# Kernel optimization log

Hardware: AMD Instinct MI355X
Metric: run time of the kernel (lower is better)

Reference implementation:

```python
import jax, jax.numpy as jnp
import numpy as np

B, T, N, D, H, F, L, V = 4, 512, 1024, 384, 8, 1536, 6, 8000
HD = D // H


def _pe(t, d):
    pos = np.arange(t)[:, None].astype(np.float32)
    div = np.exp(np.arange(0, d, 2).astype(np.float32) * (-np.log(10000.0) / d))
    pe = np.zeros((t, d), np.float32)
    pe[:, 0::2] = np.sin(pos * div)
    pe[:, 1::2] = np.cos(pos * div)
    return jnp.asarray(pe)


def _ln(x, g, b, eps=1e-5):
    m = jnp.mean(x, -1, keepdims=True)
    v = jnp.mean((x - m) ** 2, -1, keepdims=True)
    return (x - m) * jax.lax.rsqrt(v + eps) * g + b


def _mha(xq, xkv, qw, qb, kw, kb, vw, vb, ow, ob, causal):
    Bq, Tq, Dm = xq.shape
    Nk = xkv.shape[1]

    def proj(x, w, b):
        return (x @ w + b).reshape(x.shape[0], x.shape[1], H, HD).transpose(0, 2, 1, 3)

    q, k, v = proj(xq, qw, qb), proj(xkv, kw, kb), proj(xkv, vw, vb)
    s = jnp.einsum('bhtd,bhnd->bhtn', q, k) * (HD ** -0.5)
    if causal:  # triu(ones(T, T_total), diagonal=1) since T_total == T (no cache)
        mask = jnp.triu(jnp.ones((Tq, Nk), bool), 1)
        s = jnp.where(mask, -jnp.inf, s)
    p = jax.nn.softmax(s, -1)
    o = jnp.einsum('bhtn,bhnd->bhtd', p, v).transpose(0, 2, 1, 3).reshape(Bq, Tq, Dm)
    return o @ ow + ob


def setup_inputs() -> dict:
    key = jax.random.key(0)
    ks = iter(jax.random.split(key, 40))
    w = lambda shape, s=0.02: jax.random.normal(next(ks), shape, jnp.float32) * s
    inp = {
        'encoder_out': jax.random.normal(next(ks), (B, N, D), jnp.float32),
        'emb': w((V, D)),
    }
    for p in ('sa', 'ca'):
        for n in ('q', 'k', 'v', 'o'):
            inp[f'{p}_{n}w'] = w((L, D, D))
            inp[f'{p}_{n}b'] = jnp.zeros((L, D), jnp.float32)
    for n in ('ln1', 'ln2', 'ln3'):
        inp[f'{n}_g'] = jnp.ones((L, D), jnp.float32)
        inp[f'{n}_b'] = jnp.zeros((L, D), jnp.float32)
    inp['ffn_w1'] = w((L, D, F)); inp['ffn_b1'] = jnp.zeros((L, F), jnp.float32)
    inp['ffn_w2'] = w((L, F, D)); inp['ffn_b2'] = jnp.zeros((L, D), jnp.float32)
    inp['on_g'] = jnp.ones((D,), jnp.float32); inp['on_b'] = jnp.zeros((D,), jnp.float32)
    inp['out_w'] = w((D, V)); inp['out_b'] = jnp.zeros((V,), jnp.float32)
    inp['target_ids'] = jax.random.randint(next(ks), (B, T), 0, V)
    return inp


def _forward(encoder_out, emb, sa_qw, sa_qb, sa_kw, sa_kb, sa_vw, sa_vb, sa_ow, sa_ob,
             ca_qw, ca_qb, ca_kw, ca_kb, ca_vw, ca_vb, ca_ow, ca_ob,
             ln1_g, ln1_b, ln2_g, ln2_b, ln3_g, ln3_b,
             ffn_w1, ffn_b1, ffn_w2, ffn_b2, on_g, on_b, out_w, out_b, target_ids):
    x = emb[target_ids] + _pe(T, D)[None]  # [B,T,D]
    for i in range(L):
        a = _mha(x, x, sa_qw[i], sa_qb[i], sa_kw[i], sa_kb[i], sa_vw[i], sa_vb[i], sa_ow[i], sa_ob[i], True)
        x = _ln(x + a, ln1_g[i], ln1_b[i])
        c = _mha(x, encoder_out, ca_qw[i], ca_qb[i], ca_kw[i], ca_kb[i], ca_vw[i], ca_vb[i], ca_ow[i], ca_ob[i], False)
        x = _ln(x + c, ln2_g[i], ln2_b[i])
        h = jax.nn.gelu(x @ ffn_w1[i] + ffn_b1[i], approximate=False) @ ffn_w2[i] + ffn_b2[i]
        x = _ln(x + h, ln3_g[i], ln3_b[i])
    x = _ln(x, on_g, on_b)
    return x @ out_w + out_b  # logits [B,T,V]


def reference(encoder_out, emb, sa_qw, sa_qb, sa_kw, sa_kb, sa_vw, sa_vb, sa_ow, sa_ob,
              ca_qw, ca_qb, ca_kw, ca_kb, ca_vw, ca_vb, ca_ow, ca_ob,
              ln1_g, ln1_b, ln2_g, ln2_b, ln3_g, ln3_b,
              ffn_w1, ffn_b1, ffn_w2, ffn_b2, on_g, on_b, out_w, out_b, target_ids):
    return _forward(encoder_out, emb, sa_qw, sa_qb, sa_kw, sa_kb, sa_vw, sa_vb, sa_ow, sa_ob,
                    ca_qw, ca_qb, ca_kw, ca_kb, ca_vw, ca_vb, ca_ow, ca_ob,
                    ln1_g, ln1_b, ln2_g, ln2_b, ln3_g, ln3_b,
                    ffn_w1, ffn_b1, ffn_w2, ffn_b2, on_g, on_b, out_w, out_b, target_ids)
```

## Files before the change

### kernel.cpp

```cpp
#include <hip/hip_runtime.h>
#include <hip/hip_bf16.h>
#include <math.h>

typedef __hip_bfloat16 bf16;
typedef __attribute__((ext_vector_type(8))) short short8;
typedef __attribute__((ext_vector_type(4))) float f32x4;
typedef __attribute__((ext_vector_type(4))) unsigned short us4;

#define Bc 4
#define Tc 512
#define Nc 1024
#define Dc 384
#define Hc 8
#define Fc 1536
#define Lc 6
#define Vc 8000
#define HDc 48

__device__ __forceinline__ float ldsel(const void* p, long long i, int isbf) {
  return isbf ? __bfloat162float(((const bf16*)p)[i]) : ((const float*)p)[i];
}
__device__ __forceinline__ void stsel(void* p, long long i, float v, int isbf) {
  if (isbf) ((bf16*)p)[i] = __float2bfloat16(v);
  else      ((float*)p)[i] = v;
}
__device__ __forceinline__ unsigned short f2bf(float x) {
  unsigned int u = __float_as_uint(x);
  return (unsigned short)((u + 0x7fffu + ((u >> 16) & 1u)) >> 16);
}

__device__ __forceinline__ int xcd_swz(int d, int nwg) {
  const int q = nwg >> 3, r = nwg & 7;
  const int x = d & 7, idx = d >> 3;
  return (x < r) ? x * (q + 1) + idx : r * (q + 1) + (x - r) * q + idx;
}

__global__ void detect_kernel(const unsigned int* __restrict__ g,
                              int* __restrict__ flag) {
  if (threadIdx.x == 0 && blockIdx.x == 0)
    *flag = (g[0] == 0x3F803F80u) ? 1 : 0;
}

__global__ __launch_bounds__(256) void wt_kernel(
    const void* __restrict__ in, bf16* __restrict__ out, int K, int N,
    long long outStride, const int* __restrict__ flagp) {
  const int isbf = *flagp;
  __shared__ float t[32][33];
  const long long cin = (long long)blockIdx.z * K * N;
  const long long cout = (long long)blockIdx.z * outStride;
  const int n0 = blockIdx.x * 32, k0 = blockIdx.y * 32;
  const int tx = threadIdx.x, ty = threadIdx.y;
#pragma unroll
  for (int r = 0; r < 4; ++r)
    t[ty * 4 + r][tx] =
        ldsel(in, cin + (long long)(k0 + ty * 4 + r) * N + n0 + tx, isbf);
  __syncthreads();
#pragma unroll
  for (int r = 0; r < 4; ++r)
    out[cout + (long long)(n0 + ty * 4 + r) * K + k0 + tx] =
        __float2bfloat16(t[tx][ty * 4 + r]);
}

__global__ __launch_bounds__(256) void cvt_kernel(
    const void* __restrict__ in, bf16* __restrict__ out,
    const int* __restrict__ flagp) {
  const int isbf = *flagp;
  const long long i = ((long long)blockIdx.x * 256 + threadIdx.x) * 4;
  if (isbf) {
    *(us4*)((unsigned short*)out + i) = *(const us4*)((const unsigned short*)in + i);
  } else {
    float4 v = *(const float4*)((const float*)in + i);
    unsigned short* o = (unsigned short*)out + i;
    o[0] = f2bf(v.x); o[1] = f2bf(v.y); o[2] = f2bf(v.z); o[3] = f2bf(v.w);
  }
}

__global__ __launch_bounds__(256) void bfuse_kernel(
    const void* __restrict__ b0, const void* __restrict__ b1,
    const void* __restrict__ b2, float* __restrict__ out, int nseg,
    const int* __restrict__ flagp) {
  const int isbf = *flagp;
  const int i = blockIdx.x;
  for (int n = threadIdx.x; n < Dc; n += 256) {
    out[(long long)i * nseg * Dc + n] = ldsel(b0, (long long)i * Dc + n, isbf);
    if (nseg > 1)
      out[(long long)i * nseg * Dc + Dc + n] = ldsel(b1, (long long)i * Dc + n, isbf);
    if (nseg > 2)
      out[(long long)i * nseg * Dc + 2 * Dc + n] = ldsel(b2, (long long)i * Dc + n, isbf);
  }
}

template <int BN>
__global__ __launch_bounds__(256) void mgemm128_kernel(
    const bf16* __restrict__ A, const bf16* __restrict__ Bt, long long bOff,
    const void* __restrict__ bias, long long biasOff, void* __restrict__ C,
    int M, int N, int K, int cMode, int act, int biasBf,
    const int* __restrict__ flagp) {
  constexpr int RN = BN / 32;
  const int isbf = *flagp;
  const int cbf = (cMode == 2) ? isbf : cMode;
  const int bbf = (biasBf == 2) ? isbf : biasBf;

  __shared__ __align__(16) unsigned short As[128][72];
  __shared__ __align__(16) unsigned short Bs[BN][72];

  const int tid = threadIdx.x;
  const int gx = gridDim.x;
  const int wl = xcd_swz(blockIdx.y * gx + blockIdx.x, gx * gridDim.y);
  const int m0 = (wl % gx) * 128, n0 = (wl / gx) * BN;
  const int lane = tid & 63, wv = tid >> 6;
  const int wm = wv >> 1, wn = wv & 1;
  const int fr = lane & 15;
  const int fk = (lane >> 4) * 8;

  const int ar = tid >> 3;
  const int ac = (tid & 7) * 8;
  const bf16* Ap = A + (long long)(m0 + ar) * K + ac;
  const bf16* Bp_r[RN * 2];
#pragma unroll
  for (int r = 0; r < RN * 2; ++r) {
    int rn = n0 + ar + 32 * r;
    rn = (rn < N) ? rn : (N - 1);
    Bp_r[r] = Bt + bOff + (long long)rn * K + ac;
  }

  short8 pa[4], pb[RN * 2];
#pragma unroll
  for (int r = 0; r < 4; ++r) pa[r] = *(const short8*)(Ap + r * 32 * K);
#pragma unroll
  for (int r = 0; r < RN * 2; ++r) pb[r] = *(const short8*)(Bp_r[r]);

  f32x4 acc[4][RN] = {};

  for (int k0 = 0; k0 < K; k0 += 64) {
#pragma unroll
    for (int r = 0; r < 4; ++r) *(short8*)(&As[ar + 32 * r][ac]) = pa[r];
#pragma unroll
    for (int r = 0; r < RN * 2; ++r) *(short8*)(&Bs[ar + 32 * r][ac]) = pb[r];
    __syncthreads();
    if (k0 + 64 < K) {
#pragma unroll
      for (int r = 0; r < 4; ++r)
        pa[r] = *(const short8*)(Ap + r * 32 * K + k0 + 64);
#pragma unroll
      for (int r = 0; r < RN * 2; ++r)
        pb[r] = *(const short8*)(Bp_r[r] + k0 + 64);
    }
#pragma unroll
    for (int ks = 0; ks < 64; ks += 32) {
      short8 af[4];
#pragma unroll
      for (int mi = 0; mi < 4; ++mi)
        af[mi] = *(const short8*)(&As[wm * 64 + mi * 16 + fr][ks + fk]);
      short8 bg[RN];
#pragma unroll
      for (int ni = 0; ni < RN; ++ni)
        bg[ni] = *(const short8*)(&Bs[wn * (BN / 2) + ni * 16 + fr][ks + fk]);
#pragma unroll
      for (int mi = 0; mi < 4; ++mi)
#pragma unroll
        for (int ni = 0; ni < RN; ++ni)
          acc[mi][ni] =
              __builtin_amdgcn_mfma_f32_16x16x32_bf16(af[mi], bg[ni], acc[mi][ni], 0, 0, 0);
    }
    __syncthreads();
  }

#pragma unroll
  for (int ni = 0; ni < RN; ++ni) {
    const int col = n0 + wn * (BN / 2) + ni * 16 + fr;
    if (col >= N) continue;
    const float bv = bias ? ldsel(bias, biasOff + col, bbf) : 0.f;
#pragma unroll
    for (int mi = 0; mi < 4; ++mi) {
#pragma unroll
      for (int q = 0; q < 4; ++q) {
        const int row = m0 + wm * 64 + mi * 16 + (lane >> 4) * 4 + q;
        float v = acc[mi][ni][q] + bv;
        if (act == 1) v = 0.5f * v * (1.f + erff(v * 0.70710678118654752f));
        stsel(C, (long long)row * N + col, v, cbf);
      }
    }
  }
}

__global__ __launch_bounds__(256) void mgemm_kernel(
    const bf16* __restrict__ A, const void* __restrict__ B, long long bOff,
    const void* __restrict__ bias, long long biasOff, void* __restrict__ C,
    int M, int N, int K, int cMode, int act, int biasBf, int bT,
    const int* __restrict__ flagp) {
  const int isbf = *flagp;
  const int cbf = (cMode == 2) ? isbf : cMode;
  const int bbf = (biasBf == 2) ? isbf : biasBf;

  __shared__ __align__(16) unsigned short As[64][72];
  __shared__ __align__(16) unsigned short Bs[64][72];

  const int tid = threadIdx.x;
  const int gx = gridDim.x;
  const int wl = xcd_swz(blockIdx.y * gx + blockIdx.x, gx * gridDim.y);
  const int m0 = (wl % gx) * 64, n0 = (wl / gx) * 64;
  const int lane = tid & 63, wv = tid >> 6;
  const int fr = lane & 15;
  const int fk = (lane >> 4) * 8;

  const int sr = tid >> 2;
  const int sk = (tid & 3) * 16;

  f32x4 acc[4] = {};

  if (bT == 0) {
    const bf16* Bp = (const bf16*)B + bOff;
    const bf16* Ar = A + (long long)(m0 + sr) * K + sk;
    const bf16* Br = Bp + (long long)(n0 + sr) * K + sk;
    short8 a0 = *(const short8*)(Ar);
    short8 a1 = *(const short8*)(Ar + 8);
    short8 b0 = *(const short8*)(Br);
    short8 b1 = *(const short8*)(Br + 8);
    for (int k0 = 0; k0 < K; k0 += 64) {
      *(short8*)(&As[sr][sk]) = a0;
      *(short8*)(&As[sr][sk + 8]) = a1;
      *(short8*)(&Bs[sr][sk]) = b0;
      *(short8*)(&Bs[sr][sk + 8]) = b1;
      __syncthreads();
      if (k0 + 64 < K) {
        a0 = *(const short8*)(Ar + k0 + 64);
        a1 = *(const short8*)(Ar + k0 + 72);
        b0 = *(const short8*)(Br + k0 + 64);
        b1 = *(const short8*)(Br + k0 + 72);
      }
#pragma unroll
      for (int ks = 0; ks < 64; ks += 32) {
        short8 a = *(const short8*)(&As[16 * wv + fr][ks + fk]);
#pragma unroll
        for (int j = 0; j < 4; ++j) {
          short8 b = *(const short8*)(&Bs[16 * j + fr][ks + fk]);
          acc[j] = __builtin_amdgcn_mfma_f32_16x16x32_bf16(a, b, acc[j], 0, 0, 0);
        }
      }
      __syncthreads();
    }
  } else {
    const int bk = tid >> 2;
    const int bn = (tid & 3) * 16;
    for (int k0 = 0; k0 < K; k0 += 64) {
      {
        const long long off = (long long)(m0 + sr) * K + k0 + sk;
        const short8* p = (const short8*)(A + off);
        *(short8*)(&As[sr][sk]) = p[0];
        *(short8*)(&As[sr][sk + 8]) = p[1];
      }
      const long long off = bOff + (long long)(k0 + bk) * N + n0 + bn;
      if (isbf) {
        const short8* p = (const short8*)((const bf16*)B + off);
        short8 v0 = p[0], v1 = p[1];
#pragma unroll
        for (int j = 0; j < 8; ++j) {
          Bs[bn + j][bk] = (unsigned short)v0[j];
          Bs[bn + 8 + j][bk] = (unsigned short)v1[j];
        }
      } else {
        const float4* p = (const float4*)((const float*)B + off);
        float4 f0 = p[0], f1 = p[1], f2 = p[2], f3 = p[3];
        Bs[bn + 0][bk] = f2bf(f0.x);  Bs[bn + 1][bk] = f2bf(f0.y);
        Bs[bn + 2][bk] = f2bf(f0.z);  Bs[bn + 3][bk] = f2bf(f0.w);
        Bs[bn + 4][bk] = f2bf(f1.x);  Bs[bn + 5][bk] = f2bf(f1.y);
        Bs[bn + 6][bk] = f2bf(f1.z);  Bs[bn + 7][bk] = f2bf(f1.w);
        Bs[bn + 8][bk] = f2bf(f2.x);  Bs[bn + 9][bk] = f2bf(f2.y);
        Bs[bn + 10][bk] = f2bf(f2.z); Bs[bn + 11][bk] = f2bf(f2.w);
        Bs[bn + 12][bk] = f2bf(f3.x); Bs[bn + 13][bk] = f2bf(f3.y);
        Bs[bn + 14][bk] = f2bf(f3.z); Bs[bn + 15][bk] = f2bf(f3.w);
      }
      __syncthreads();
#pragma unroll
      for (int ks = 0; ks < 64; ks += 32) {
        short8 a = *(const short8*)(&As[16 * wv + fr][ks + fk]);
#pragma unroll
        for (int j = 0; j < 4; ++j) {
          short8 b = *(const short8*)(&Bs[16 * j + fr][ks + fk]);
          acc[j] = __builtin_amdgcn_mfma_f32_16x16x32_bf16(a, b, acc[j], 0, 0, 0);
        }
      }
      __syncthreads();
    }
  }

#pragma unroll
  for (int j = 0; j < 4; ++j) {
    const int col = n0 + 16 * j + fr;
    float bv = bias ? ldsel(bias, biasOff + col, bbf) : 0.f;
#pragma unroll
    for (int q = 0; q < 4; ++q) {
      const int row = m0 + 16 * wv + (lane >> 4) * 4 + q;
      float v = acc[j][q] + bv;
      if (act == 1) v = 0.5f * v * (1.f + erff(v * 0.70710678118654752f));
      stsel(C, (long long)row * N + col, v, cbf);
    }
  }
}

__global__ __launch_bounds__(256) void mattn_kernel(
    const bf16* __restrict__ Qb, int ldq, const bf16* __restrict__ Kb,
    const bf16* __restrict__ Vb, int ldkv, int kvRows,
    float* __restrict__ PO, float* __restrict__ Mb, float* __restrict__ Lb,
    int Nk, int causal) {
  const int bh = blockIdx.y;
  const int b = bh >> 3, h = bh & 7;
  const int row0 = blockIdx.x * 64;
  const int z = blockIdx.z;
  const int tid = threadIdx.x;
  const int lane = tid & 63, wv = tid >> 6;
  const int fr = lane & 15, g = lane >> 4;
  const int fk = g * 8, g4 = g * 4;
  const int rbase = row0 + wv * 16 + g4;

  __shared__ __align__(16) unsigned short Ks[64][72];
  __shared__ __align__(16) unsigned short Vt[48][72];
  __shared__ __align__(16) unsigned short Ps[4][16][72];

  for (int i = tid; i < 64 * 16; i += 256) Ks[i >> 4][48 + (i & 15)] = 0;

  const int qrow = row0 + wv * 16 + fr;
  const bf16* Qp = Qb + (long long)(b * Tc + qrow) * ldq + h * HDc;
  short8 q0 = *(const short8*)(Qp + fk);
  short8 q1 = {};
  if (g < 2) q1 = *(const short8*)(Qp + 32 + fk);

  const bf16* Kp = Kb + (long long)b * kvRows * ldkv + h * HDc;
  const bf16* Vp = Vb + (long long)b * kvRows * ldkv + h * HDc;

  const int c0 = tid, c1 = 256 + tid;
  const int r0 = c0 / 6, o0 = (c0 % 6) * 8;
  const int r1 = c1 / 6, o1 = (c1 % 6) * 8;
  const bool has1 = (tid < 128);

  const int nT = causal ? (blockIdx.x + 1) : (Nk >> 6);
  const int tlo = (nT * z) >> 1, thi = (nT * (z + 1)) >> 1;

  float m[4] = {-3e38f, -3e38f, -3e38f, -3e38f};
  float l[4] = {0.f, 0.f, 0.f, 0.f};
  f32x4 oa[3] = {};

  short8 kA = {}, vA = {}, kB = {}, vB = {};
  if (tlo < thi) {
    const long long nb = (long long)tlo * 64;
    kA = *(const short8*)(Kp + (nb + r0) * ldkv + o0);
    vA = *(const short8*)(Vp + (nb + r0) * ldkv + o0);
    if (has1) {
      kB = *(const short8*)(Kp + (nb + r1) * ldkv + o1);
      vB = *(const short8*)(Vp + (nb + r1) * ldkv + o1);
    }
  }

  const float scale = 0.20823509f;

  for (int t = tlo; t < thi; ++t) {
    *(short8*)&Ks[r0][o0] = kA;
#pragma unroll
    for (int j = 0; j < 8; ++j) Vt[o0 + j][r0] = (unsigned short)vA[j];
    if (has1) {
      *(short8*)&Ks[r1][o1] = kB;
#pragma unroll
      for (int j = 0; j < 8; ++j) Vt[o1 + j][r1] = (unsigned short)vB[j];
    }
    __syncthreads();

    if (t + 1 < thi) {
      const long long nb = (long long)(t + 1) * 64;
      kA = *(const short8*)(Kp + (nb + r0) * ldkv + o0);
      vA = *(const short8*)(Vp + (nb + r0) * ldkv + o0);
      if (has1) {
        kB = *(const short8*)(Kp + (nb + r1) * ldkv + o1);
        vB = *(const short8*)(Vp + (nb + r1) * ldkv + o1);
      }
    }

    f32x4 s[4] = {};
#pragma unroll
    for (int tt = 0; tt < 4; ++tt) {
      short8 b0 = *(const short8*)&Ks[16 * tt + fr][fk];
      short8 b1 = *(const short8*)&Ks[16 * tt + fr][32 + fk];
      s[tt] = __builtin_amdgcn_mfma_f32_16x16x32_bf16(q0, b0, s[tt], 0, 0, 0);
      s[tt] = __builtin_amdgcn_mfma_f32_16x16x32_bf16(q1, b1, s[tt], 0, 0, 0);
    }

    const int n0 = t * 64;
#pragma unroll
    for (int tt = 0; tt < 4; ++tt) {
      const int n = n0 + 16 * tt + fr;
#pragma unroll
      for (int q = 0; q < 4; ++q) {
        float v = s[tt][q] * scale;
        if (causal && n > rbase + q) v = -3e38f;
        s[tt][q] = v;
      }
    }

#pragma unroll
    for (int q = 0; q < 4; ++q) {
      float tm = fmaxf(fmaxf(s[0][q], s[1][q]), fmaxf(s[2][q], s[3][q]));
      tm = fmaxf(tm, __shfl_xor(tm, 1, 64));
      tm = fmaxf(tm, __shfl_xor(tm, 2, 64));
      tm = fmaxf(tm, __shfl_xor(tm, 4, 64));
      tm = fmaxf(tm, __shfl_xor(tm, 8, 64));
      const float mn = fmaxf(m[q], tm);
      const float f = exp2f(m[q] - mn);
      float rs = 0.f;
#pragma unroll
      for (int tt = 0; tt < 4; ++tt) {
        float p = exp2f(s[tt][q] - mn);
        s[tt][q] = p;
        rs += p;
      }
      rs += __shfl_xor(rs, 1, 64);
      rs += __shfl_xor(rs, 2, 64);
      rs += __shfl_xor(rs, 4, 64);
      rs += __shfl_xor(rs, 8, 64);
      l[q] = l[q] * f + rs;
      m[q] = mn;
      oa[0][q] *= f;
      oa[1][q] *= f;
      oa[2][q] *= f;
    }

#pragma unroll
    for (int tt = 0; tt < 4; ++tt)
#pragma unroll
      for (int q = 0; q < 4; ++q)
        Ps[wv][g4 + q][16 * tt + fr] = f2bf(s[tt][q]);

#pragma unroll
    for (int ks = 0; ks < 64; ks += 32) {
      short8 a = *(const short8*)&Ps[wv][fr][ks + fk];
#pragma unroll
      for (int jd = 0; jd < 3; ++jd) {
        short8 bv = *(const short8*)&Vt[16 * jd + fr][ks + fk];
        oa[jd] = __builtin_amdgcn_mfma_f32_16x16x32_bf16(a, bv, oa[jd], 0, 0, 0);
      }
    }
    __syncthreads();
  }

#pragma unroll
  for (int q = 0; q < 4; ++q) {
    float* pp = PO + (long long)(z * (Bc * Tc) + b * Tc + rbase + q) * Dc + h * HDc;
#pragma unroll
    for (int jd = 0; jd < 3; ++jd) pp[16 * jd + fr] = oa[jd][q];
    if (fr == 0) {
      const int mi = z * (Bc * Hc * Tc) + (bh << 9) + rbase + q;
      Mb[mi] = m[q];
      Lb[mi] = l[q];
    }
  }
}

__global__ __launch_bounds__(384) void acomb_kernel(
    const float* __restrict__ PO, const float* __restrict__ Mb,
    const float* __restrict__ Lb, bf16* __restrict__ ATT) {
  const int row = blockIdx.x;
  const int d = threadIdx.x;
  const int b = row >> 9, t = row & 511;
  const int h = d / HDc;
  const int mi = ((b << 3) + h) * Tc + t;
  const float m0 = Mb[mi], m1 = Mb[Bc * Hc * Tc + mi];
  const float l0 = Lb[mi], l1 = Lb[Bc * Hc * Tc + mi];
  const float M = fmaxf(m0, m1);
  const float w0 = exp2f(m0 - M), w1 = exp2f(m1 - M);
  const float L = w0 * l0 + w1 * l1;
  const float o = (w0 * PO[(long long)row * Dc + d] +
                   w1 * PO[(long long)(Bc * Tc + row) * Dc + d]) / L;
  ATT[(long long)row * Dc + d] = __float2bfloat16(o);
}

__global__ __launch_bounds__(256) void lnw_kernel(
    const float* __restrict__ X, const float* __restrict__ R,
    const void* __restrict__ g, const void* __restrict__ bta, long long gOff,
    void* __restrict__ Y, int yMode, bf16* __restrict__ Yb,
    const int* __restrict__ flagp) {
  const int isbf = *flagp;
  const long long row = blockIdx.x * 4 + (threadIdx.x >> 6);
  const int lane = threadIdx.x & 63;
  const float* xr = X + row * Dc;
  const float* rr = R ? R + row * Dc : nullptr;
  float v[6];
  float s = 0.f, s2 = 0.f;
#pragma unroll
  for (int j = 0; j < 6; ++j) {
    const int d = lane + 64 * j;
    float x = xr[d] + (rr ? rr[d] : 0.f);
    v[j] = x; s += x; s2 += x * x;
  }
#pragma unroll
  for (int k = 1; k < 64; k <<= 1) {
    s += __shfl_xor(s, k, 64);
    s2 += __shfl_xor(s2, k, 64);
  }
  const float mean = s * (1.f / 384.f);
  const float var = s2 * (1.f / 384.f) - mean * mean;
  const float rstd = rsqrtf(var + 1e-5f);
  const long long yo = row * Dc;
#pragma unroll
  for (int j = 0; j < 6; ++j) {
    const int d = lane + 64 * j;
    float y = (v[j] - mean) * rstd * ldsel(g, gOff + d, isbf) +
              ldsel(bta, gOff + d, isbf);
    stsel(Y, yo + d, y, yMode);
    if (Yb) Yb[yo + d] = __float2bfloat16(y);
  }
}

__global__ __launch_bounds__(384) void embed_kernel(
    const void* __restrict__ emb, const int* __restrict__ ids,
    float* __restrict__ X, bf16* __restrict__ Xb,
    const int* __restrict__ flagp) {
  const int isbf = *flagp;
  long long row = blockIdx.x;
  int t = (int)(row % Tc);
  int d = threadIdx.x;
  int id = ids[row];
  float e = ldsel(emb, (long long)id * Dc + d, isbf);
  int i2 = d & ~1;
  float div = expf((float)i2 * (-9.210340371976184f / 384.f));
  float ang = (float)t * div;
  float pe = (d & 1) ? cosf(ang) : sinf(ang);
  float v = e + pe;
  X[row * Dc + d] = v;
  Xb[row * Dc + d] = __float2bfloat16(v);
}

extern "C" void kernel_launch(void* const* d_in, const int* in_sizes, int n_in,
                              void* d_out, int out_size, void* d_ws,
                              size_t ws_size, hipStream_t stream) {
  (void)in_sizes; (void)n_in; (void)out_size;

  const void* enc = d_in[0];
  const void* emb = d_in[1];
  const void* sa_w[4]; const void* sa_b[4];
  for (int j = 0; j < 4; ++j) { sa_w[j] = d_in[2 + 2 * j]; sa_b[j] = d_in[3 + 2 * j]; }
  const void* ca_w[4]; const void* ca_b[4];
  for (int j = 0; j < 4; ++j) { ca_w[j] = d_in[10 + 2 * j]; ca_b[j] = d_in[11 + 2 * j]; }
  const void* ln_g[3]; const void* ln_b[3];
  for (int j = 0; j < 3; ++j) { ln_g[j] = d_in[18 + 2 * j]; ln_b[j] = d_in[19 + 2 * j]; }
  const void* fw1 = d_in[24];
  const void* fb1 = d_in[25];
  const void* fw2 = d_in[26];
  const void* fb2 = d_in[27];
  const void* ong = d_in[28];
  const void* onb = d_in[29];
  const void* outw = d_in[30];
  const void* outb = d_in[31];
  const int* ids = (const int*)d_in[32];

  char* ob = (char*)d_out;
  float* X   = (float*)ob;
  bf16* Xb   = (bf16*)(ob + 3145728);
  float* AO  = (float*)(ob + 4718592);
  bf16* QKV  = (bf16*)(ob + 7864320);
  bf16* KVca = (bf16*)(ob + 12582912);
  bf16* ATT  = (bf16*)(ob + 18874368);
  bf16* HID  = (bf16*)(ob + 20447232);
  float* PO  = (float*)(ob + 20447232);
  float* Mb  = (float*)(ob + 26738688);
  float* Lb  = (float*)(ob + 26869760);
  bf16* encB = (bf16*)(ob + 27000832);
  float* bQKV = (float*)(ob + 30146560);
  float* bKVc = (float*)(ob + 30174208);

  bf16* Y = (bf16*)d_ws;
  int* flag = (int*)((char*)d_ws + 1572864);

  const bool bigws = (ws_size >= (size_t)36028672);
  char* wtb = (char*)d_ws + 1573120;
  bf16* saQKVT = (bf16*)(wtb + 0);
  bf16* saOT   = (bf16*)(wtb + 5308416);
  bf16* caQT   = (bf16*)(wtb + 7077888);
  bf16* caKVT  = (bf16*)(wtb + 8847360);
  bf16* caOT   = (bf16*)(wtb + 12386304);
  bf16* f1T    = (bf16*)(wtb + 14155776);
  bf16* f2T    = (bf16*)(wtb + 21233664);
  bf16* outT   = (bf16*)(wtb + 28311552);

  const int BT = Bc * Tc;
  const int F32 = 0, BF16 = 1, FLAG = 2;

  detect_kernel<<<dim3(1), dim3(64), 0, stream>>>((const unsigned int*)ln_g[0], flag);

  if (bigws) {
    auto wt = [&](const void* in, bf16* out, int K, int N, long long ostr, int C) {
      wt_kernel<<<dim3(N / 32, K / 32, C), dim3(32, 8), 0, stream>>>(
          in, out, K, N, ostr, flag);
    };
    wt(sa_w[0], saQKVT, 384, 384, 1152LL * 384, Lc);
    wt(sa_w[1], saQKVT + 147456, 384, 384, 1152LL * 384, Lc);
    wt(sa_w[2], saQKVT + 294912, 384, 384, 1152LL * 384, Lc);
    wt(sa_w[3], saOT, 384, 384, 147456, Lc);
    wt(ca_w[0], caQT, 384, 384, 147456, Lc);
    wt(ca_w[1], caKVT, 384, 384, 294912, Lc);
    wt(ca_w[2], caKVT + 147456, 384, 384, 294912, Lc);
    wt(ca_w[3], caOT, 384, 384, 147456, Lc);
    wt(fw1, f1T, 384, 1536, 589824, Lc);
    wt(fw2, f2T, 1536, 384, 589824, Lc);
    wt(outw, outT, 384, 8000, 0, 1);
    bfuse_kernel<<<dim3(Lc), dim3(256), 0, stream>>>(sa_b[0], sa_b[1], sa_b[2],
                                                     bQKV, 3, flag);
    bfuse_kernel<<<dim3(Lc), dim3(256), 0, stream>>>(ca_b[1], ca_b[2], ca_b[2],
                                                     bKVc, 2, flag);
  }
  cvt_kernel<<<dim3(1536), dim3(256), 0, stream>>>(enc, encB, flag);

  auto gemmBig = [&](const bf16* A, const bf16* Bt, long long bOff,
                     const void* bias, long long biasOff, int biasBf, void* C,
                     int M, int N, int K, int cM, int act) {
    mgemm128_kernel<128>
        <<<dim3(M / 128, (N + 127) / 128), dim3(256), 0, stream>>>(
            A, Bt, bOff, bias, biasOff, C, M, N, K, cM, act, biasBf, flag);
  };
  auto gemmT = [&](const bf16* A, const bf16* Bt, long long bOff,
                   const void* bias, long long biasOff, int biasBf, void* C,
                   int M, int N, int K, int cM, int act) {
    mgemm_kernel<<<dim3(M / 64, N / 64), dim3(256), 0, stream>>>(
        A, Bt, bOff, bias, biasOff, C, M, N, K, cM, act, biasBf, 0, flag);
  };
  auto gemmO = [&](const bf16* A, const void* Bo, long long bOff,
                   const void* bias, long long biasOff, void* C,
                   int M, int N, int K, int cM, int act) {
    mgemm_kernel<<<dim3(M / 64, N / 64), dim3(256), 0, stream>>>(
        A, Bo, bOff, bias, biasOff, C, M, N, K, cM, act, FLAG, 1, flag);
  };
  auto ln = [&](const float* Xp, const float* Rp, const void* g,
                const void* b, long long gOff, void* Yp, int yMode, bf16* Yb) {
    lnw_kernel<<<dim3(BT / 4), dim3(256), 0, stream>>>(Xp, Rp, g, b, gOff, Yp,
                                                       yMode, Yb, flag);
  };
  auto attn = [&](const bf16* Q, int ldq, const bf16* Kp, const bf16* Vp,
                  int ldkv, int kvRows, int Nk, int causal) {
    mattn_kernel<<<dim3(Tc / 64, Bc * Hc, 2), dim3(256), 0, stream>>>(
        Q, ldq, Kp, Vp, ldkv, kvRows, PO, Mb, Lb, Nk, causal);
    acomb_kernel<<<dim3(BT), dim3(384), 0, stream>>>(PO, Mb, Lb, ATT);
  };

  embed_kernel<<<dim3(BT), dim3(384), 0, stream>>>(emb, ids, X, Xb, flag);

  bf16* Qf = QKV;
  bf16* Kf = KVca;
  bf16* Vf = (bf16*)((char*)KVca + 3145728);

  for (int i = 0; i < Lc; ++i) {
    const long long wD = (long long)i * Dc * Dc;
    const long long bD = (long long)i * Dc;

    if (bigws) {
      gemmT(Xb, saQKVT, (long long)i * 1152 * 384, bQKV, (long long)i * 1152,
            F32, QKV, BT, 1152, 384, BF16, 0);
      attn(QKV, 1152, QKV + 384, QKV + 768, 1152, Tc, Tc, 1);
      gemmT(ATT, saOT, wD, sa_b[3], bD, FLAG, AO, BT, Dc, Dc, F32, 0);
    } else {
      gemmO(Xb, sa_w[0], wD, sa_b[0], bD, Qf, BT, Dc, Dc, BF16, 0);
      gemmO(Xb, sa_w[1], wD, sa_b[1], bD, Kf, BT, Dc, Dc, BF16, 0);
      gemmO(Xb, sa_w[2], wD, sa_b[2], bD, Vf, BT, Dc, Dc, BF16, 0);
      attn(Qf, 384, Kf, Vf, 384, Tc, Tc, 1);
      gemmO(ATT, sa_w[3], wD, sa_b[3], bD, AO, BT, Dc, Dc, F32, 0);
    }
    ln(X, AO, ln_g[0], ln_b[0], bD, X, F32, Xb);

    if (bigws) {
      gemmT(Xb, caQT, wD, ca_b[0], bD, FLAG, QKV, BT, Dc, Dc, BF16, 0);
      gemmT(encB, caKVT, (long long)i * 768 * 384, bKVc, (long long)i * 768,
            F32, KVca, Bc * Nc, 768, 384, BF16, 0);
      attn(QKV, 384, KVca, KVca + 384, 768, Nc, Nc, 0);
      gemmT(ATT, caOT, wD, ca_b[3], bD, FLAG, AO, BT, Dc, Dc, F32, 0);
    } else {
      gemmO(Xb, ca_w[0], wD, ca_b[0], bD, Qf, BT, Dc, Dc, BF16, 0);
      gemmO(encB, ca_w[1], wD, ca_b[1], bD, Kf, Bc * Nc, Dc, Dc, BF16, 0);
      gemmO(encB, ca_w[2], wD, ca_b[2], bD, Vf, Bc * Nc, Dc, Dc, BF16, 0);
      attn(Qf, 384, Kf, Vf, 384, Nc, Nc, 0);
      gemmO(ATT, ca_w[3], wD, ca_b[3], bD, AO, BT, Dc, Dc, F32, 0);
    }
    ln(X, AO, ln_g[1], ln_b[1], bD, X, F32, Xb);

    if (bigws) {
      gemmT(Xb, f1T, (long long)i * 1536 * 384, fb1, (long long)i * Fc, FLAG,
            HID, BT, Fc, Dc, BF16, 1 );
      gemmT(HID, f2T, (long long)i * 384 * 1536, fb2, bD, FLAG, AO,
            BT, Dc, Fc, F32, 0);
    } else {
      gemmO(Xb, fw1, (long long)i * Dc * Fc, fb1, (long long)i * Fc, HID,
            BT, Fc, Dc, BF16, 1);
      gemmO(HID, fw2, (long long)i * Fc * Dc, fb2, bD, AO, BT, Dc, Fc, F32, 0);
    }
    ln(X, AO, ln_g[2], ln_b[2], bD, X, F32, Xb);
  }

  ln(X, nullptr, ong, onb, 0, Y, BF16, nullptr);
  if (bigws)
    gemmBig(Y, outT, 0, outb, 0, FLAG, d_out, BT, Vc, Dc, FLAG, 0);
  else
    gemmO(Y, outw, 0, outb, 0, d_out, BT, Vc, Dc, FLAG, 0);
}
```

Baseline: 1.070 ms.

## Split-K narrow GEMMs, 4-way attention KV split, smaller output GEMM tile

Adds split-K to the 64x64 GEMM kernel through Klen/Ktot/kOff parameters. The N=384 projection and FFN-down GEMMs become two half-K launches into separate fp32 buffers, and the layernorm kernel sums both partials. Attention now splits the KV range four ways instead of two, with partials stored in reused scratch slots and a 4-way combine. The vocab GEMM switches to a 64-wide N tile to launch more blocks. The aim is better CU occupancy for small grids, at the cost of extra launches, more fp32 partial traffic and more scratch-buffer aliasing.

```diff
diff --git a/kernel.cpp b/kernel.cpp
--- a/kernel.cpp
+++ b/kernel.cpp
@@ -187,8 +187,8 @@
 __global__ __launch_bounds__(256) void mgemm_kernel(
     const bf16* __restrict__ A, const void* __restrict__ B, long long bOff,
     const void* __restrict__ bias, long long biasOff, void* __restrict__ C,
-    int M, int N, int K, int cMode, int act, int biasBf, int bT,
-    const int* __restrict__ flagp) {
+    int M, int N, int Klen, int Ktot, int kOff, int cMode, int act, int biasBf,
+    int bT, const int* __restrict__ flagp) {
   const int isbf = *flagp;
   const int cbf = (cMode == 2) ? isbf : cMode;
   const int bbf = (biasBf == 2) ? isbf : biasBf;
@@ -211,19 +211,19 @@
 
   if (bT == 0) {
     const bf16* Bp = (const bf16*)B + bOff;
-    const bf16* Ar = A + (long long)(m0 + sr) * K + sk;
-    const bf16* Br = Bp + (long long)(n0 + sr) * K + sk;
+    const bf16* Ar = A + (long long)(m0 + sr) * Ktot + kOff + sk;
+    const bf16* Br = Bp + (long long)(n0 + sr) * Ktot + kOff + sk;
     short8 a0 = *(const short8*)(Ar);
     short8 a1 = *(const short8*)(Ar + 8);
     short8 b0 = *(const short8*)(Br);
     short8 b1 = *(const short8*)(Br + 8);
-    for (int k0 = 0; k0 < K; k0 += 64) {
+    for (int k0 = 0; k0 < Klen; k0 += 64) {
       *(short8*)(&As[sr][sk]) = a0;
       *(short8*)(&As[sr][sk + 8]) = a1;
       *(short8*)(&Bs[sr][sk]) = b0;
       *(short8*)(&Bs[sr][sk + 8]) = b1;
       __syncthreads();
-      if (k0 + 64 < K) {
+      if (k0 + 64 < Klen) {
         a0 = *(const short8*)(Ar + k0 + 64);
         a1 = *(const short8*)(Ar + k0 + 72);
         b0 = *(const short8*)(Br + k0 + 64);
@@ -243,14 +243,14 @@
   } else {
     const int bk = tid >> 2;
     const int bn = (tid & 3) * 16;
-    for (int k0 = 0; k0 < K; k0 += 64) {
+    for (int k0 = 0; k0 < Klen; k0 += 64) {
       {
-        const long long off = (long long)(m0 + sr) * K + k0 + sk;
+        const long long off = (long long)(m0 + sr) * Ktot + kOff + k0 + sk;
         const short8* p = (const short8*)(A + off);
         *(short8*)(&As[sr][sk]) = p[0];
         *(short8*)(&As[sr][sk + 8]) = p[1];
       }
-      const long long off = bOff + (long long)(k0 + bk) * N + n0 + bn;
+      const long long off = bOff + (long long)(kOff + k0 + bk) * N + n0 + bn;
       if (isbf) {
         const short8* p = (const short8*)((const bf16*)B + off);
         short8 v0 = p[0], v1 = p[1];
@@ -302,7 +302,8 @@
 __global__ __launch_bounds__(256) void mattn_kernel(
     const bf16* __restrict__ Qb, int ldq, const bf16* __restrict__ Kb,
     const bf16* __restrict__ Vb, int ldkv, int kvRows,
-    float* __restrict__ PO, float* __restrict__ Mb, float* __restrict__ Lb,
+    float* __restrict__ P0s, float* __restrict__ P1s, float* __restrict__ P2s,
+    float* __restrict__ P3s, float* __restrict__ Mb, float* __restrict__ Lb,
     int Nk, int causal) {
   const int bh = blockIdx.y;
   const int b = bh >> 3, h = bh & 7;
@@ -335,7 +336,7 @@
   const bool has1 = (tid < 128);
 
   const int nT = causal ? (blockIdx.x + 1) : (Nk >> 6);
-  const int tlo = (nT * z) >> 1, thi = (nT * (z + 1)) >> 1;
+  const int tlo = (nT * z) >> 2, thi = (nT * (z + 1)) >> 2;
 
   float m[4] = {-3e38f, -3e38f, -3e38f, -3e38f};
   float l[4] = {0.f, 0.f, 0.f, 0.f};
@@ -441,9 +442,10 @@
     __syncthreads();
   }
 
+  float* Pz = (z == 0) ? P0s : (z == 1) ? P1s : (z == 2) ? P2s : P3s;
 #pragma unroll
   for (int q = 0; q < 4; ++q) {
-    float* pp = PO + (long long)(z * (Bc * Tc) + b * Tc + rbase + q) * Dc + h * HDc;
+    float* pp = Pz + (long long)(b * Tc + rbase + q) * Dc + h * HDc;
 #pragma unroll
     for (int jd = 0; jd < 3; ++jd) pp[16 * jd + fr] = oa[jd][q];
     if (fr == 0) {
@@ -455,39 +457,43 @@
 }
 
 __global__ __launch_bounds__(384) void acomb_kernel(
-    const float* __restrict__ PO, const float* __restrict__ Mb,
-    const float* __restrict__ Lb, bf16* __restrict__ ATT) {
+    const float* __restrict__ P0s, const float* __restrict__ P1s,
+    const float* __restrict__ P2s, const float* __restrict__ P3s,
+    const float* __restrict__ Mb, const float* __restrict__ Lb,
+    bf16* __restrict__ ATT) {
   const int row = blockIdx.x;
   const int d = threadIdx.x;
   const int b = row >> 9, t = row & 511;
   const int h = d / HDc;
   const int mi = ((b << 3) + h) * Tc + t;
-  const float m0 = Mb[mi], m1 = Mb[Bc * Hc * Tc + mi];
-  const float l0 = Lb[mi], l1 = Lb[Bc * Hc * Tc + mi];
-  const float M = fmaxf(m0, m1);
+  const int S = Bc * Hc * Tc;
+  const float m0 = Mb[mi], m1 = Mb[S + mi], m2 = Mb[2 * S + mi], m3 = Mb[3 * S + mi];
+  const float M = fmaxf(fmaxf(m0, m1), fmaxf(m2, m3));
   const float w0 = exp2f(m0 - M), w1 = exp2f(m1 - M);
-  const float L = w0 * l0 + w1 * l1;
-  const float o = (w0 * PO[(long long)row * Dc + d] +
-                   w1 * PO[(long long)(Bc * Tc + row) * Dc + d]) / L;
-  ATT[(long long)row * Dc + d] = __float2bfloat16(o);
+  const float w2 = exp2f(m2 - M), w3 = exp2f(m3 - M);
+  const float L = w0 * Lb[mi] + w1 * Lb[S + mi] + w2 * Lb[2 * S + mi] + w3 * Lb[3 * S + mi];
+  const long long off = (long long)row * Dc + d;
+  const float o = (w0 * P0s[off] + w1 * P1s[off] + w2 * P2s[off] + w3 * P3s[off]) / L;
+  ATT[off] = __float2bfloat16(o);
 }
 
 __global__ __launch_bounds__(256) void lnw_kernel(
     const float* __restrict__ X, const float* __restrict__ R,
-    const void* __restrict__ g, const void* __restrict__ bta, long long gOff,
-    void* __restrict__ Y, int yMode, bf16* __restrict__ Yb,
-    const int* __restrict__ flagp) {
+    const float* __restrict__ R1, const void* __restrict__ g,
+    const void* __restrict__ bta, long long gOff, void* __restrict__ Y,
+    int yMode, bf16* __restrict__ Yb, const int* __restrict__ flagp) {
   const int isbf = *flagp;
   const long long row = blockIdx.x * 4 + (threadIdx.x >> 6);
   const int lane = threadIdx.x & 63;
   const float* xr = X + row * Dc;
   const float* rr = R ? R + row * Dc : nullptr;
+  const float* rr1 = R1 ? R1 + row * Dc : nullptr;
   float v[6];
   float s = 0.f, s2 = 0.f;
 #pragma unroll
   for (int j = 0; j < 6; ++j) {
     const int d = lane + 64 * j;
-    float x = xr[d] + (rr ? rr[d] : 0.f);
+    float x = xr[d] + (rr ? rr[d] : 0.f) + (rr1 ? rr1[d] : 0.f);
     v[j] = x; s += x; s2 += x * x;
   }
 #pragma unroll
@@ -559,12 +565,18 @@
   bf16* KVca = (bf16*)(ob + 12582912);
   bf16* ATT  = (bf16*)(ob + 18874368);
   bf16* HID  = (bf16*)(ob + 20447232);
-  float* PO  = (float*)(ob + 20447232);
-  float* Mb  = (float*)(ob + 26738688);
-  float* Lb  = (float*)(ob + 26869760);
   bf16* encB = (bf16*)(ob + 27000832);
   float* bQKV = (float*)(ob + 30146560);
   float* bKVc = (float*)(ob + 30174208);
+  float* Mb  = (float*)(ob + 30192640);
+  float* Lb  = (float*)(ob + 30454784);
+  const size_t SLOT = 3145728;
+  float* sHID0 = (float*)(ob + 20447232);
+  float* sHID1 = (float*)(ob + 20447232 + SLOT);
+  float* sKV0  = (float*)(ob + 12582912);
+  float* sKV1  = (float*)(ob + 12582912 + SLOT);
+  float* sAO   = AO;
+  float* sQKVt = (float*)(ob + 7864320 + 1572864);
 
   bf16* Y = (bf16*)d_ws;
   int* flag = (int*)((char*)d_ws + 1572864);
@@ -611,39 +623,42 @@
   auto gemmBig = [&](const bf16* A, const bf16* Bt, long long bOff,
                      const void* bias, long long biasOff, int biasBf, void* C,
                      int M, int N, int K, int cM, int act) {
-    mgemm128_kernel<128>
-        <<<dim3(M / 128, (N + 127) / 128), dim3(256), 0, stream>>>(
-            A, Bt, bOff, bias, biasOff, C, M, N, K, cM, act, biasBf, flag);
+    mgemm128_kernel<64><<<dim3(M / 128, (N + 63) / 64), dim3(256), 0, stream>>>(
+        A, Bt, bOff, bias, biasOff, C, M, N, K, cM, act, biasBf, flag);
   };
   auto gemmT = [&](const bf16* A, const bf16* Bt, long long bOff,
                    const void* bias, long long biasOff, int biasBf, void* C,
-                   int M, int N, int K, int cM, int act) {
+                   int M, int N, int Klen, int Ktot, int kOff, int cM, int act) {
     mgemm_kernel<<<dim3(M / 64, N / 64), dim3(256), 0, stream>>>(
-        A, Bt, bOff, bias, biasOff, C, M, N, K, cM, act, biasBf, 0, flag);
+        A, Bt, bOff, bias, biasOff, C, M, N, Klen, Ktot, kOff, cM, act, biasBf,
+        0, flag);
   };
   auto gemmO = [&](const bf16* A, const void* Bo, long long bOff,
                    const void* bias, long long biasOff, void* C,
                    int M, int N, int K, int cM, int act) {
     mgemm_kernel<<<dim3(M / 64, N / 64), dim3(256), 0, stream>>>(
-        A, Bo, bOff, bias, biasOff, C, M, N, K, cM, act, FLAG, 1, flag);
+        A, Bo, bOff, bias, biasOff, C, M, N, K, K, 0, cM, act, FLAG, 1, flag);
   };
-  auto ln = [&](const float* Xp, const float* Rp, const void* g,
-                const void* b, long long gOff, void* Yp, int yMode, bf16* Yb) {
-    lnw_kernel<<<dim3(BT / 4), dim3(256), 0, stream>>>(Xp, Rp, g, b, gOff, Yp,
-                                                       yMode, Yb, flag);
+  auto ln = [&](const float* Xp, const float* Rp, const float* R1p,
+                const void* g, const void* b, long long gOff, void* Yp,
+                int yMode, bf16* Yb) {
+    lnw_kernel<<<dim3(BT / 4), dim3(256), 0, stream>>>(Xp, Rp, R1p, g, b, gOff,
+                                                       Yp, yMode, Yb, flag);
   };
   auto attn = [&](const bf16* Q, int ldq, const bf16* Kp, const bf16* Vp,
-                  int ldkv, int kvRows, int Nk, int causal) {
-    mattn_kernel<<<dim3(Tc / 64, Bc * Hc, 2), dim3(256), 0, stream>>>(
-        Q, ldq, Kp, Vp, ldkv, kvRows, PO, Mb, Lb, Nk, causal);
-    acomb_kernel<<<dim3(BT), dim3(384), 0, stream>>>(PO, Mb, Lb, ATT);
+                  int ldkv, int kvRows, int Nk, int causal, float* P0,
+                  float* P1, float* P2, float* P3) {
+    mattn_kernel<<<dim3(Tc / 64, Bc * Hc, 4), dim3(256), 0, stream>>>(
+        Q, ldq, Kp, Vp, ldkv, kvRows, P0, P1, P2, P3, Mb, Lb, Nk, causal);
+    acomb_kernel<<<dim3(BT), dim3(384), 0, stream>>>(P0, P1, P2, P3, Mb, Lb,
+                                                     ATT);
   };
 
   embed_kernel<<<dim3(BT), dim3(384), 0, stream>>>(emb, ids, X, Xb, flag);
 
   bf16* Qf = QKV;
   bf16* Kf = KVca;
-  bf16* Vf = (bf16*)((char*)KVca + 3145728);
+  bf16* Vf = (bf16*)((char*)KVca + SLOT);
 
   for (int i = 0; i < Lc; ++i) {
     const long long wD = (long long)i * Dc * Dc;
@@ -651,47 +666,56 @@
 
     if (bigws) {
       gemmT(Xb, saQKVT, (long long)i * 1152 * 384, bQKV, (long long)i * 1152,
-            F32, QKV, BT, 1152, 384, BF16, 0);
-      attn(QKV, 1152, QKV + 384, QKV + 768, 1152, Tc, Tc, 1);
-      gemmT(ATT, saOT, wD, sa_b[3], bD, FLAG, AO, BT, Dc, Dc, F32, 0);
+            F32, QKV, BT, 1152, 384, 384, 0, BF16, 0);
+      attn(QKV, 1152, QKV + 384, QKV + 768, 1152, Tc, Tc, 1,
+           sKV0, sKV1, sHID0, sHID1);
+      gemmT(ATT, saOT, wD, sa_b[3], bD, FLAG, AO, BT, Dc, 192, 384, 0, F32, 0);
+      gemmT(ATT, saOT, wD, nullptr, 0, F32, sHID0, BT, Dc, 192, 384, 192, F32, 0);
+      ln(X, AO, sHID0, ln_g[0], ln_b[0], bD, X, F32, Xb);
     } else {
       gemmO(Xb, sa_w[0], wD, sa_b[0], bD, Qf, BT, Dc, Dc, BF16, 0);
       gemmO(Xb, sa_w[1], wD, sa_b[1], bD, Kf, BT, Dc, Dc, BF16, 0);
       gemmO(Xb, sa_w[2], wD, sa_b[2], bD, Vf, BT, Dc, Dc, BF16, 0);
-      attn(Qf, 384, Kf, Vf, 384, Tc, Tc, 1);
+      attn(Qf, 384, Kf, Vf, 384, Tc, Tc, 1, sHID0, sHID1, sAO, sQKVt);
       gemmO(ATT, sa_w[3], wD, sa_b[3], bD, AO, BT, Dc, Dc, F32, 0);
-    }
-    ln(X, AO, ln_g[0], ln_b[0], bD, X, F32, Xb);
+      ln(X, AO, nullptr, ln_g[0], ln_b[0], bD, X, F32, Xb);
+    }
 
     if (bigws) {
-      gemmT(Xb, caQT, wD, ca_b[0], bD, FLAG, QKV, BT, Dc, Dc, BF16, 0);
+      gemmT(Xb, caQT, wD, ca_b[0], bD, FLAG, QKV, BT, Dc, 384, 384, 0, BF16, 0);
       gemmT(encB, caKVT, (long long)i * 768 * 384, bKVc, (long long)i * 768,
-            F32, KVca, Bc * Nc, 768, 384, BF16, 0);
-      attn(QKV, 384, KVca, KVca + 384, 768, Nc, Nc, 0);
-      gemmT(ATT, caOT, wD, ca_b[3], bD, FLAG, AO, BT, Dc, Dc, F32, 0);
+            F32, KVca, Bc * Nc, 768, 384, 384, 0, BF16, 0);
+      attn(QKV, 384, KVca, KVca + 384, 768, Nc, Nc, 0,
+           sHID0, sHID1, sAO, sQKVt);
+      gemmT(ATT, caOT, wD, ca_b[3], bD, FLAG, AO, BT, Dc, 192, 384, 0, F32, 0);
+      gemmT(ATT, caOT, wD, nullptr, 0, F32, sHID0, BT, Dc, 192, 384, 192, F32, 0);
+      ln(X, AO, sHID0, ln_g[1], ln_b[1], bD, X, F32, Xb);
     } else {
       gemmO(Xb, ca_w[0], wD, ca_b[0], bD, Qf, BT, Dc, Dc, BF16, 0);
       gemmO(encB, ca_w[1], wD, ca_b[1], bD, Kf, Bc * Nc, Dc, Dc, BF16, 0);
       gemmO(encB, ca_w[2], wD, ca_b[2], bD, Vf, Bc * Nc, Dc, Dc, BF16, 0);
-      attn(Qf, 384, Kf, Vf, 384, Nc, Nc, 0);
+      attn(Qf, 384, Kf, Vf, 384, Nc, Nc, 0, sHID0, sHID1, sAO, sQKVt);
       gemmO(ATT, ca_w[3], wD, ca_b[3], bD, AO, BT, Dc, Dc, F32, 0);
-    }
-    ln(X, AO, ln_g[1], ln_b[1], bD, X, F32, Xb);
+      ln(X, AO, nullptr, ln_g[1], ln_b[1], bD, X, F32, Xb);
+    }
 
     if (bigws) {
       gemmT(Xb, f1T, (long long)i * 1536 * 384, fb1, (long long)i * Fc, FLAG,
-            HID, BT, Fc, Dc, BF16, 1 );
+            HID, BT, Fc, 384, 384, 0, BF16, 1 );
       gemmT(HID, f2T, (long long)i * 384 * 1536, fb2, bD, FLAG, AO,
-            BT, Dc, Fc, F32, 0);
+            BT, Dc, 768, 1536, 0, F32, 0);
+      gemmT(HID, f2T, (long long)i * 384 * 1536, nullptr, 0, F32, sKV0,
+            BT, Dc, 768, 1536, 768, F32, 0);
+      ln(X, AO, sKV0, ln_g[2], ln_b[2], bD, X, F32, Xb);
     } else {
       gemmO(Xb, fw1, (long long)i * Dc * Fc, fb1, (long long)i * Fc, HID,
             BT, Fc, Dc, BF16, 1);
       gemmO(HID, fw2, (long long)i * Fc * Dc, fb2, bD, AO, BT, Dc, Fc, F32, 0);
-    }
-    ln(X, AO, ln_g[2], ln_b[2], bD, X, F32, Xb);
-  }
-
-  ln(X, nullptr, ong, onb, 0, Y, BF16, nullptr);
+      ln(X, AO, nullptr, ln_g[2], ln_b[2], bD, X, F32, Xb);
+    }
+  }
+
+  ln(X, nullptr, nullptr, ong, onb, 0, Y, BF16, nullptr);
   if (bigws)
     gemmBig(Y, outT, 0, outb, 0, FLAG, d_out, BT, Vc, Dc, FLAG, 0);
   else
```

New measurement: 1.159 ms. +8.3%, slower.
